# Kernel tuning notes

Hardware: AMD Instinct MI355X
Metric: run time of the kernel (lower is better)

The kernel has to match this reference:

```python
import jax, jax.numpy as jnp
import numpy as np

ACTION_NS = [3, 3, 2, 4, 24]        # forward_back, left_right, jump, sneak_sprint, attack_...
RANGE_STARTS = [6, 8, 10, 11, 14]   # action_ranges starts (indices 0..5 are commit + camera ops)
N_ACTIONS = 37
LOGIT_DIM = 36
MIN_DELTA = 0.5 / 2**3
MAX_STEP = 20
MAX_CAMSTEP = 6
B, NUM_INPUT, HIDDEN = 32768, 1024, 2048
D_IN = NUM_INPUT + 4 + LOGIT_DIM


def setup_inputs():
    key = jax.random.key(0)
    ks = jax.random.split(key, 12)
    inp = {
        "fc_input": jax.random.normal(ks[0], (B, NUM_INPUT), jnp.float32),
        "camera": jax.random.normal(ks[1], (B, 2), jnp.float32),
        "rand_u": jax.random.uniform(ks[2], (B,), jnp.float32),
        "W1": (jax.random.normal(ks[3], (D_IN, HIDDEN), jnp.float32) / np.sqrt(D_IN)).astype(jnp.float32),
        "b1": jnp.zeros((HIDDEN,), jnp.float32),
        "W2": (jax.random.normal(ks[4], (HIDDEN, N_ACTIONS), jnp.float32) / np.sqrt(HIDDEN)).astype(jnp.float32),
        "b2": jnp.zeros((N_ACTIONS,), jnp.float32),
    }
    names = ["act_fb", "act_lr", "act_jp", "act_ss", "act_atk"]
    for i, (nm, n) in enumerate(zip(names, ACTION_NS)):
        inp[nm] = jax.random.randint(ks[5 + i], (B,), 0, n, jnp.int32)
    return inp


def _discretize_scan(camera, acts):
    # Faithful jax version of the 20-step no_grad target/input construction loop.
    nB = camera.shape[0]
    cam0, cam1 = camera[:, 0], camera[:, 1]

    def step(carry, _):
        ac, delta, rdac, dch, cam_steps, committed, norm = carry
        oh = [jax.nn.one_hot(r, n, dtype=jnp.float32) for r, n in zip(rdac, ACTION_NS)]
        inp_vec = jnp.concatenate([ac] + oh + [delta[:, None], dch.astype(jnp.float32)[:, None]], axis=1)  # [B,40]
        norm = norm + (~committed).astype(jnp.float32)
        commit = ((jnp.abs(cam0) < 1e-5) & (jnp.abs(cam1) < 1e-5)) | (cam_steps >= MAX_CAMSTEP)
        for r, a in zip(rdac, acts):
            commit = commit & (r == a)
        dac = jnp.zeros((nB,), jnp.int32)
        modified = commit
        new_rdac = []
        for r, a, rs in zip(rdac, acts, RANGE_STARTS):
            disc = (~modified) & (r != a)
            dac = jnp.where(disc & (a == 0), r - 1 + rs, jnp.where(disc, a - 1 + rs, dac))
            new_rdac.append(jnp.where(disc, a, r))
            modified = modified | disc
        d2 = delta * 2.0
        # NOTE: original torch code compares cam[:,1] against ac[:,0]; bug preserved.
        dmask = (~modified) & (~dch) & ((jnp.abs(cam0 - ac[:, 0]) > d2) | (jnp.abs(cam1 - ac[:, 0]) > d2))
        dac = jnp.where(dmask, 5, dac)
        delta = jnp.where(dmask, jnp.clip(d2, -0.5, 0.5), delta)
        modified = modified | dmask
        sx = jnp.where(cam0 < ac[:, 0], -1.0, 1.0)
        sy = jnp.where(cam1 < ac[:, 1], -1.0, 1.0)
        quad = jnp.where(sx < 0, jnp.where(sy < 0, 1, 3), jnp.where(sy < 0, 2, 4)).astype(jnp.int32)
        dac = jnp.where(~modified, quad, dac)
        move = jnp.stack([sx, sy], axis=1) * delta[:, None]
        ac = jnp.where((~modified)[:, None], ac + move, ac)
        delta = jnp.where(~modified, delta * 0.5, delta)
        dch = dch | (~modified)
        cam_steps = cam_steps + (~modified).astype(jnp.int32)
        committed = committed | commit
        return (ac, delta, tuple(new_rdac), dch, cam_steps, committed, norm), (inp_vec, dac)

    init = (jnp.zeros((nB, 2), jnp.float32),
            jnp.full((nB,), MIN_DELTA, jnp.float32),
            tuple(jnp.zeros((nB,), jnp.int32) for _ in ACTION_NS),
            jnp.zeros((nB,), bool),
            jnp.zeros((nB,), jnp.int32),
            jnp.zeros((nB,), bool),
            jnp.zeros((nB,), jnp.float32))
    carry, (all_inputs, all_dacs) = jax.lax.scan(step, init, None, length=MAX_STEP)
    return all_inputs, all_dacs, carry[-1]  # [T,B,40], [T,B], norm [B]


def reference(fc_input, camera, rand_u, W1, b1, W2, b2, act_fb, act_lr, act_jp, act_ss, act_atk):
    acts = (act_fb, act_lr, act_jp, act_ss, act_atk)
    all_inputs, all_dacs, norm = _discretize_scan(camera, acts)
    rand_sam = jnp.minimum((rand_u * norm).astype(jnp.int32), MAX_STEP - 1)  # sample an uncommitted step
    idx = jnp.arange(fc_input.shape[0])
    sel = jax.lax.stop_gradient(all_inputs[rand_sam, idx])  # [B,40]
    tgt = jax.lax.stop_gradient(all_dacs[rand_sam, idx])    # [B]
    x = jnp.concatenate([fc_input, sel], axis=1)
    h = x @ W1 + b1
    h = h * jax.nn.sigmoid(h)  # swish
    logits = h @ W2 + b2
    logp = jax.nn.log_softmax(logits, axis=-1)
    loss = -jnp.take_along_axis(logp, tgt[:, None], axis=1)[:, 0]  # per-sample CE (reduction='none')
    return loss
```

## Files before the change

kernel.cpp:

```cpp
#include <hip/hip_runtime.h>
#include <hip/hip_bf16.h>
#include <stdint.h>

#define B_ROWS 32768
#define NUM_IN 1024
#define D_PAD2 1088
#define HID    2048
#define NPAD   64

typedef __attribute__((ext_vector_type(8))) short bf16x8;
typedef __attribute__((ext_vector_type(4))) float f32x4;
typedef unsigned short ushort_t;

__device__ __forceinline__ unsigned short f2bf(float f){
  union { float f; uint32_t u; } x; x.f = f;
  uint32_t u = x.u;
  return (unsigned short)((u + 0x7FFFu + ((u >> 16) & 1u)) >> 16);
}

__device__ __forceinline__ void gload16(const void* g, void* l){
  __builtin_amdgcn_global_load_lds((const __attribute__((address_space(1))) void*)g,
                                   (__attribute__((address_space(3))) void*)l, 16, 0, 0);
}

__device__ __forceinline__ int disc_step(
    float cam0, float cam1, const int a[5],
    float& ac0, float& ac1, float& delta,
    int r[5], bool& dch, int& cam_steps, bool& committed, float& norm)
{
  const int RS[5] = {6, 8, 10, 11, 14};
  norm += committed ? 0.0f : 1.0f;
  bool commit = ((fabsf(cam0) < 1e-5f) && (fabsf(cam1) < 1e-5f)) || (cam_steps >= 6);
  #pragma unroll
  for (int i = 0; i < 5; ++i) commit = commit && (r[i] == a[i]);
  int dac = 0;
  bool modified = commit;
  #pragma unroll
  for (int i = 0; i < 5; ++i){
    bool disc = (!modified) && (r[i] != a[i]);
    if (disc){
      dac = (a[i] == 0) ? (r[i] - 1 + RS[i]) : (a[i] - 1 + RS[i]);
      r[i] = a[i];
      modified = true;
    }
  }
  float d2 = delta * 2.0f;
  bool dmask = (!modified) && (!dch) &&
               ((fabsf(cam0 - ac0) > d2) || (fabsf(cam1 - ac0) > d2));
  if (dmask){ dac = 5; delta = fminf(d2, 0.5f); modified = true; }
  if (!modified){
    float sx = (cam0 < ac0) ? -1.0f : 1.0f;
    float sy = (cam1 < ac1) ? -1.0f : 1.0f;
    dac = (sx < 0.0f) ? ((sy < 0.0f) ? 1 : 3) : ((sy < 0.0f) ? 2 : 4);
    ac0 += sx * delta; ac1 += sy * delta;
    delta *= 0.5f;
    dch = true;
    cam_steps += 1;
  }
  committed = committed || commit;
  return dac;
}

__global__ void k_prep(const float* __restrict__ fc, const float* __restrict__ W1,
                       const float* __restrict__ W2,
                       const float* __restrict__ camera, const float* __restrict__ rand_u,
                       const int* __restrict__ afb, const int* __restrict__ alr,
                       const int* __restrict__ ajp, const int* __restrict__ ass,
                       const int* __restrict__ aat,
                       unsigned short* __restrict__ xb, unsigned short* __restrict__ w1t,
                       unsigned short* __restrict__ w2t, int* __restrict__ tgt)
{
  const int b = blockIdx.x;
  const int tid = threadIdx.x;
  if (b < 16384){
    int gid = b * 256 + tid;
    int row = gid >> 7;
    int c   = gid & 127;
    const float4* p = (const float4*)(fc + (size_t)row * NUM_IN + c * 8);
    float4 f0 = p[0], f1 = p[1];
    uint4 pk;
    pk.x = (uint32_t)f2bf(f0.x) | ((uint32_t)f2bf(f0.y) << 16);
    pk.y = (uint32_t)f2bf(f0.z) | ((uint32_t)f2bf(f0.w) << 16);
    pk.z = (uint32_t)f2bf(f1.x) | ((uint32_t)f2bf(f1.y) << 16);
    pk.w = (uint32_t)f2bf(f1.z) | ((uint32_t)f2bf(f1.w) << 16);
    *(uint4*)(xb + (size_t)row * D_PAD2 + c * 8) = pk;
    return;
  }
  if (b < 25088){
    int idx = (b - 16384) * 256 + tid;
    int n = idx / D_PAD2;
    int k = idx - n * D_PAD2;
    float v = (k < 1064) ? W1[(size_t)k * HID + n] : 0.0f;
    w1t[idx] = f2bf(v);
    return;
  }
  if (b < 25600){
    int idx = (b - 25088) * 256 + tid;
    int n = idx >> 11;
    int k = idx & (HID - 1);
    float v = (n < 37) ? W2[(size_t)k * 37 + n] : 0.0f;
    w2t[idx] = f2bf(v);
    return;
  }
  int row = (b - 25600) * 256 + tid;
  float cam0 = camera[2*row], cam1 = camera[2*row + 1];
  int a[5] = { afb[row], alr[row], ajp[row], ass[row], aat[row] };

  float ac0 = 0.f, ac1 = 0.f, delta = 0.0625f, norm = 0.f;
  int r[5] = {0,0,0,0,0};
  bool dch = false, committed = false; int cam_steps = 0;
  for (int t = 0; t < 20; ++t)
    disc_step(cam0, cam1, a, ac0, ac1, delta, r, dch, cam_steps, committed, norm);

  int rs = (int)(rand_u[row] * norm);
  if (rs > 19) rs = 19;
  if (rs < 0) rs = 0;

  ac0 = 0.f; ac1 = 0.f; delta = 0.0625f; norm = 0.f;
  r[0]=r[1]=r[2]=r[3]=r[4]=0; dch = false; committed = false; cam_steps = 0;
  for (int t = 0; t < rs; ++t)
    disc_step(cam0, cam1, a, ac0, ac1, delta, r, dch, cam_steps, committed, norm);

  float vec[40];
  #pragma unroll
  for (int j = 0; j < 40; ++j) vec[j] = 0.0f;
  vec[0] = ac0; vec[1] = ac1;
  const int offs[5] = {2, 5, 8, 10, 14};
  #pragma unroll
  for (int i = 0; i < 5; ++i) vec[offs[i] + r[i]] = 1.0f;
  vec[38] = delta; vec[39] = dch ? 1.0f : 0.0f;

  int dac = disc_step(cam0, cam1, a, ac0, ac1, delta, r, dch, cam_steps, committed, norm);
  tgt[row] = dac;

  unsigned short* o = xb + (size_t)row * D_PAD2 + NUM_IN;
  #pragma unroll
  for (int j = 0; j < 40; ++j) o[j] = f2bf(vec[j]);
  #pragma unroll
  for (int j = 40; j < 64; ++j) o[j] = 0;
}

#define LDS_A0 0
#define LDS_A1 16384
#define LDS_B0 32768
#define LDS_B1 49152

#define STAGE(G, REG, ROW0, KT, HALF) do { \
    const ushort_t* s0_ = (G) + (size_t)((ROW0) + (HALF)*128 + srow) * D_PAD2 + ((KT) << 6) + scol; \
    gload16(s0_, lds + (REG) + (HALF)*8192 + t*8); \
    gload16(s0_ + (size_t)64 * D_PAD2, lds + (REG) + (HALF)*8192 + 4096 + t*8); \
  } while(0)

#define LDA_(REG, MH) do { \
    _Pragma("unroll") for (int mi_ = 0; mi_ < 4; ++mi_){ \
      const int row_ = arow_base + (MH)*64 + mi_*16; \
      _Pragma("unroll") for (int kk_ = 0; kk_ < 2; ++kk_) \
        aR[mi_][kk_] = *(const bf16x8*)(lds + (REG) + row_*64 + (((kk_*4+lg)^axor)<<3)); \
    } \
  } while(0)

#define LDB_(REG, NH, BR) do { \
    _Pragma("unroll") for (int ni_ = 0; ni_ < 2; ++ni_){ \
      const int row_ = brow_base + (NH)*32 + ni_*16; \
      _Pragma("unroll") for (int kk_ = 0; kk_ < 2; ++kk_) \
        BR[ni_][kk_] = *(const bf16x8*)(lds + (REG) + row_*64 + (((kk_*4+lg)^axor)<<3)); \
    } \
  } while(0)

#define MMA(MH, NH, BR) do { \
    __builtin_amdgcn_s_setprio(1); \
    _Pragma("unroll") for (int mi_ = 0; mi_ < 4; ++mi_) \
    _Pragma("unroll") for (int ni_ = 0; ni_ < 2; ++ni_) \
    _Pragma("unroll") for (int kk_ = 0; kk_ < 2; ++kk_) \
      acc[(MH)*4+mi_][(NH)*2+ni_] = __builtin_amdgcn_mfma_f32_16x16x32_bf16( \
          aR[mi_][kk_], BR[ni_][kk_], acc[(MH)*4+mi_][(NH)*2+ni_], 0, 0, 0); \
    __builtin_amdgcn_s_setprio(0); \
  } while(0)

#define BAR() __builtin_amdgcn_s_barrier()
#define WAIT_LGKM0() asm volatile("s_waitcnt lgkmcnt(0)" ::: "memory")
#define WAIT_VM6()   asm volatile("s_waitcnt vmcnt(6)" ::: "memory")
#define WAIT_VM0()   asm volatile("s_waitcnt vmcnt(0)" ::: "memory")

__global__ __launch_bounds__(512, 2) void k_gemm1(const ushort_t* __restrict__ xb,
                                                  const ushort_t* __restrict__ w1t,
                                                  const ushort_t* __restrict__ w2t,
                                                  const float* __restrict__ b1,
                                                  float* __restrict__ pbuf)
{
  __shared__ ushort_t lds[65536];
  const int t = threadIdx.x;
  const int lane = t & 63;
  const int wid = t >> 6, wm = wid >> 2, wn = wid & 3;
  const int lr = lane & 15, lg = lane >> 4;

  const int bid = blockIdx.x;
  const int swz = (bid & 7) * 128 + (bid >> 3);
  const int brow = (swz >> 3) << 8;
  const int bcol = (swz & 7) << 8;

  const int srow = t >> 3;
  const int scol = ((t & 7) ^ (srow & 7)) << 3;

  const int axor = lr & 7;
  const int arow_base = wm*128 + lr;
  const int brow_base = wn*64 + lr;

  f32x4 acc[8][4] = {};
  bf16x8 aR[4][2], bR0[2][2], bR1[2][2];

  STAGE(xb,  LDS_A0, brow, 0, 0);  STAGE(xb,  LDS_A0, brow, 0, 1);
  STAGE(w1t, LDS_B0, bcol, 0, 0);  STAGE(w1t, LDS_B0, bcol, 0, 1);
  STAGE(w1t, LDS_B1, bcol, 1, 0);  STAGE(w1t, LDS_B1, bcol, 1, 1);
  STAGE(xb,  LDS_A1, brow, 1, 0);
  WAIT_VM6();
  BAR();

  for (int i = 0; i < 8; ++i){
    const int c1 = 2*i + 1;
    const int n0 = 2*i + 2;
    const int n1 = (2*i + 3 <= 16) ? 2*i + 3 : 16;

    LDA_(LDS_A0, 0); LDB_(LDS_B0, 0, bR0); LDB_(LDS_B0, 1, bR1);
    STAGE(xb, LDS_A1, brow, c1, 1);
    BAR(); WAIT_LGKM0();
    MMA(0, 0, bR0);
    BAR();
    STAGE(w1t, LDS_B0, bcol, n0, 0);
    BAR();
    MMA(0, 1, bR1);
    BAR();
    LDA_(LDS_A0, 1);
    STAGE(w1t, LDS_B0, bcol, n0, 1);
    BAR(); WAIT_LGKM0();
    MMA(1, 0, bR0);
    BAR();
    STAGE(xb, LDS_A0, brow, n0, 0);
    WAIT_VM6();
    BAR();
    MMA(1, 1, bR1);
    BAR();
    LDA_(LDS_A1, 0); LDB_(LDS_B1, 0, bR0); LDB_(LDS_B1, 1, bR1);
    STAGE(xb, LDS_A0, brow, n0, 1);
    BAR(); WAIT_LGKM0();
    MMA(0, 0, bR0);
    BAR();
    STAGE(w1t, LDS_B1, bcol, n1, 0);
    BAR();
    MMA(0, 1, bR1);
    BAR();
    LDA_(LDS_A1, 1);
    STAGE(w1t, LDS_B1, bcol, n1, 1);
    BAR(); WAIT_LGKM0();
    MMA(1, 0, bR0);
    BAR();
    STAGE(xb, LDS_A1, brow, n1, 0);
    WAIT_VM6();
    BAR();
    MMA(1, 1, bR1);
    BAR();
  }

  LDA_(LDS_A0, 0); LDB_(LDS_B0, 0, bR0); LDB_(LDS_B0, 1, bR1);
  MMA(0, 0, bR0); MMA(0, 1, bR1);
  LDA_(LDS_A0, 1);
  MMA(1, 0, bR0); MMA(1, 1, bR1);

  bf16x8 w2fA[4][4];
  #pragma unroll
  for (int ks = 0; ks < 4; ++ks)
    #pragma unroll
    for (int ni = 0; ni < 4; ++ni)
      w2fA[ks][ni] = *(const bf16x8*)(w2t + (size_t)(ni*16 + lr) * HID + bcol + ks*32 + lg*8);

  WAIT_VM0();
  BAR();

  float b1v[4];
  #pragma unroll
  for (int ni = 0; ni < 4; ++ni) b1v[ni] = b1[bcol + wn*64 + ni*16 + lr];

  #pragma unroll
  for (int mi = 0; mi < 8; ++mi){
    #pragma unroll
    for (int ni = 0; ni < 4; ++ni){
      const int col = wn*64 + ni*16 + lr;
      #pragma unroll
      for (int i2 = 0; i2 < 4; ++i2){
        const int row = wm*128 + mi*16 + lg*4 + i2;
        float v = acc[mi][ni][i2] + b1v[ni];
        float s = v / (1.0f + __expf(-v));
        const int chunk = (col >> 3) ^ (row & 7);
        lds[row*256 + chunk*8 + (col & 7)] = f2bf(s);
      }
    }
  }
  __syncthreads();

  bf16x8 w2fB[4][4];
  #pragma unroll
  for (int ks = 0; ks < 4; ++ks)
    #pragma unroll
    for (int ni = 0; ni < 4; ++ni)
      w2fB[ks][ni] = *(const bf16x8*)(w2t + (size_t)(ni*16 + lr) * HID + bcol + (ks+4)*32 + lg*8);

  const int rb = wid * 32;
  f32x4 acc2[2][4] = {};
  #pragma unroll
  for (int ks = 0; ks < 8; ++ks){
    bf16x8 a2[2];
    #pragma unroll
    for (int m = 0; m < 2; ++m){
      const int row = rb + m*16 + lr;
      a2[m] = *(const bf16x8*)(lds + row*256 + (((ks*4+lg) ^ (lr & 7)) << 3));
    }
    #pragma unroll
    for (int m = 0; m < 2; ++m)
      #pragma unroll
      for (int ni = 0; ni < 4; ++ni)
        acc2[m][ni] = __builtin_amdgcn_mfma_f32_16x16x32_bf16(
            a2[m], (ks < 4) ? w2fA[ks & 3][ni] : w2fB[ks & 3][ni], acc2[m][ni], 0, 0, 0);
  }

  const int cb = bcol >> 8;
  #pragma unroll
  for (int m = 0; m < 2; ++m)
    #pragma unroll
    for (int ni = 0; ni < 4; ++ni)
      #pragma unroll
      for (int i2 = 0; i2 < 4; ++i2){
        const int r = brow + rb + m*16 + lg*4 + i2;
        pbuf[((size_t)cb << 21) + ((size_t)r << 6) + ni*16 + lr] = acc2[m][ni][i2];
      }
}

__global__ __launch_bounds__(256) void k_red(const float* __restrict__ pbuf,
                                             const float* __restrict__ b2,
                                             const int* __restrict__ tgt,
                                             float* __restrict__ loss)
{
  const int lane = threadIdx.x & 63, w = threadIdx.x >> 6;
  const int row0 = blockIdx.x * 128 + w * 32;
  const float bias = (lane < 37) ? b2[lane] : 0.0f;
  for (int i = 0; i < 32; ++i){
    const int r = row0 + i;
    float s = 0.0f;
    #pragma unroll
    for (int cb = 0; cb < 8; ++cb)
      s += pbuf[((size_t)cb << 21) + ((size_t)r << 6) + lane];
    float x = (lane < 37) ? (s + bias) : -1e30f;
    float m = x;
    #pragma unroll
    for (int off = 1; off < 64; off <<= 1) m = fmaxf(m, __shfl_xor(m, off, 64));
    float e = __expf(x - m);
    float se = e;
    #pragma unroll
    for (int off = 1; off < 64; off <<= 1) se += __shfl_xor(se, off, 64);
    const int tg = tgt[r];
    const float pick = __shfl(x, tg, 64);
    if (lane == 0) loss[r] = m + __logf(se) - pick;
  }
}

extern "C" void kernel_launch(void* const* d_in, const int* in_sizes, int n_in,
                              void* d_out, int out_size, void* d_ws, size_t ws_size,
                              hipStream_t stream)
{
  (void)in_sizes; (void)n_in; (void)out_size; (void)ws_size;
  const float* fc  = (const float*)d_in[0];
  const float* cam = (const float*)d_in[1];
  const float* ru  = (const float*)d_in[2];
  const float* W1  = (const float*)d_in[3];
  const float* b1  = (const float*)d_in[4];
  const float* W2  = (const float*)d_in[5];
  const float* b2  = (const float*)d_in[6];
  const int* afb = (const int*)d_in[7];
  const int* alr = (const int*)d_in[8];
  const int* ajp = (const int*)d_in[9];
  const int* ass = (const int*)d_in[10];
  const int* aat = (const int*)d_in[11];
  float* loss = (float*)d_out;

  char* ws = (char*)d_ws;
  unsigned short* xb  = (unsigned short*)(ws);
  unsigned short* w1t = (unsigned short*)(ws + 71303168);
  unsigned short* w2t = (unsigned short*)(ws + 75759616);
  int*            tgt = (int*)           (ws + 76021760);
  float*          pbuf= (float*)         (ws + 76152832);

  k_prep<<<25728, 256, 0, stream>>>(fc, W1, W2, cam, ru, afb, alr, ajp, ass, aat,
                                    xb, w1t, w2t, tgt);
  k_gemm1<<<(B_ROWS/256) * (HID/256), 512, 0, stream>>>(xb, w1t, w2t, b1, pbuf);
  k_red  <<<B_ROWS / 128, 256, 0, stream>>>(pbuf, b2, tgt, loss);
}
```

Baseline: 275.6 us.

## Double-buffer GEMM1 register fragments to overlap LDS reads with MFMA

Splits the A and B operand registers into two banks and issues the LDS fragment reads for the next sub-tile before the current MFMA block runs. This replaces the explicit lgkmcnt(0) waits, so LDS read latency can hide behind matrix math, and the epilogue is reordered to match. The cost is many more live VGPRs under a 512-thread, 2-block launch bound, which risks register spills or lower occupancy. Correctness now depends on the compiler inserting the right waits before each fragment is used.

```diff
diff --git a/kernel.cpp b/kernel.cpp
--- a/kernel.cpp
+++ b/kernel.cpp
@@ -151,34 +151,34 @@
     gload16(s0_ + (size_t)64 * D_PAD2, lds + (REG) + (HALF)*8192 + 4096 + t*8); \
   } while(0)
 
-#define LDA_(REG, MH) do { \
+#define RDA(BANK, REG, MH) do { \
     _Pragma("unroll") for (int mi_ = 0; mi_ < 4; ++mi_){ \
       const int row_ = arow_base + (MH)*64 + mi_*16; \
       _Pragma("unroll") for (int kk_ = 0; kk_ < 2; ++kk_) \
-        aR[mi_][kk_] = *(const bf16x8*)(lds + (REG) + row_*64 + (((kk_*4+lg)^axor)<<3)); \
+        BANK[mi_][kk_] = *(const bf16x8*)(lds + (REG) + row_*64 + (((kk_*4+lg)^axor)<<3)); \
     } \
   } while(0)
 
-#define LDB_(REG, NH, BR) do { \
+#define RDB(BANK, REG) do { \
+    _Pragma("unroll") for (int nh_ = 0; nh_ < 2; ++nh_) \
     _Pragma("unroll") for (int ni_ = 0; ni_ < 2; ++ni_){ \
-      const int row_ = brow_base + (NH)*32 + ni_*16; \
+      const int row_ = brow_base + nh_*32 + ni_*16; \
       _Pragma("unroll") for (int kk_ = 0; kk_ < 2; ++kk_) \
-        BR[ni_][kk_] = *(const bf16x8*)(lds + (REG) + row_*64 + (((kk_*4+lg)^axor)<<3)); \
+        BANK[nh_][ni_][kk_] = *(const bf16x8*)(lds + (REG) + row_*64 + (((kk_*4+lg)^axor)<<3)); \
     } \
   } while(0)
 
-#define MMA(MH, NH, BR) do { \
+#define MMAQ(AB, MH, BB, NH) do { \
     __builtin_amdgcn_s_setprio(1); \
     _Pragma("unroll") for (int mi_ = 0; mi_ < 4; ++mi_) \
     _Pragma("unroll") for (int ni_ = 0; ni_ < 2; ++ni_) \
     _Pragma("unroll") for (int kk_ = 0; kk_ < 2; ++kk_) \
       acc[(MH)*4+mi_][(NH)*2+ni_] = __builtin_amdgcn_mfma_f32_16x16x32_bf16( \
-          aR[mi_][kk_], BR[ni_][kk_], acc[(MH)*4+mi_][(NH)*2+ni_], 0, 0, 0); \
+          AB[mi_][kk_], BB[NH][ni_][kk_], acc[(MH)*4+mi_][(NH)*2+ni_], 0, 0, 0); \
     __builtin_amdgcn_s_setprio(0); \
   } while(0)
 
 #define BAR() __builtin_amdgcn_s_barrier()
-#define WAIT_LGKM0() asm volatile("s_waitcnt lgkmcnt(0)" ::: "memory")
 #define WAIT_VM6()   asm volatile("s_waitcnt vmcnt(6)" ::: "memory")
 #define WAIT_VM0()   asm volatile("s_waitcnt vmcnt(0)" ::: "memory")
 
@@ -207,7 +207,7 @@
   const int brow_base = wn*64 + lr;
 
   f32x4 acc[8][4] = {};
-  bf16x8 aR[4][2], bR0[2][2], bR1[2][2];
+  bf16x8 aA[4][2], aB[4][2], bX[2][2][2], bY[2][2][2];
 
   STAGE(xb,  LDS_A0, brow, 0, 0);  STAGE(xb,  LDS_A0, brow, 0, 1);
   STAGE(w1t, LDS_B0, bcol, 0, 0);  STAGE(w1t, LDS_B0, bcol, 0, 1);
@@ -215,56 +215,58 @@
   STAGE(xb,  LDS_A1, brow, 1, 0);
   WAIT_VM6();
   BAR();
+  RDA(aA, LDS_A0, 0); RDB(bX, LDS_B0);
 
   for (int i = 0; i < 8; ++i){
     const int c1 = 2*i + 1;
     const int n0 = 2*i + 2;
     const int n1 = (2*i + 3 <= 16) ? 2*i + 3 : 16;
 
-    LDA_(LDS_A0, 0); LDB_(LDS_B0, 0, bR0); LDB_(LDS_B0, 1, bR1);
     STAGE(xb, LDS_A1, brow, c1, 1);
-    BAR(); WAIT_LGKM0();
-    MMA(0, 0, bR0);
+    BAR();
+    RDA(aB, LDS_A0, 1);
+    MMAQ(aA, 0, bX, 0);
     BAR();
     STAGE(w1t, LDS_B0, bcol, n0, 0);
     BAR();
-    MMA(0, 1, bR1);
-    BAR();
-    LDA_(LDS_A0, 1);
+    MMAQ(aA, 0, bX, 1);
+    BAR();
     STAGE(w1t, LDS_B0, bcol, n0, 1);
-    BAR(); WAIT_LGKM0();
-    MMA(1, 0, bR0);
+    BAR();
+    MMAQ(aB, 1, bX, 0);
     BAR();
     STAGE(xb, LDS_A0, brow, n0, 0);
     WAIT_VM6();
     BAR();
-    MMA(1, 1, bR1);
-    BAR();
-    LDA_(LDS_A1, 0); LDB_(LDS_B1, 0, bR0); LDB_(LDS_B1, 1, bR1);
+    RDA(aA, LDS_A1, 0); RDB(bY, LDS_B1);
+    MMAQ(aB, 1, bX, 1);
+    BAR();
     STAGE(xb, LDS_A0, brow, n0, 1);
-    BAR(); WAIT_LGKM0();
-    MMA(0, 0, bR0);
+    BAR();
+    RDA(aB, LDS_A1, 1);
+    MMAQ(aA, 0, bY, 0);
     BAR();
     STAGE(w1t, LDS_B1, bcol, n1, 0);
     BAR();
-    MMA(0, 1, bR1);
-    BAR();
-    LDA_(LDS_A1, 1);
+    MMAQ(aA, 0, bY, 1);
+    BAR();
     STAGE(w1t, LDS_B1, bcol, n1, 1);
-    BAR(); WAIT_LGKM0();
-    MMA(1, 0, bR0);
+    BAR();
+    MMAQ(aB, 1, bY, 0);
     BAR();
     STAGE(xb, LDS_A1, brow, n1, 0);
     WAIT_VM6();
     BAR();
-    MMA(1, 1, bR1);
-    BAR();
-  }
-
-  LDA_(LDS_A0, 0); LDB_(LDS_B0, 0, bR0); LDB_(LDS_B0, 1, bR1);
-  MMA(0, 0, bR0); MMA(0, 1, bR1);
-  LDA_(LDS_A0, 1);
-  MMA(1, 0, bR0); MMA(1, 1, bR1);
+    RDA(aA, LDS_A0, 0); RDB(bX, LDS_B0);
+    MMAQ(aB, 1, bY, 1);
+    BAR();
+  }
+
+  MMAQ(aA, 0, bX, 0);
+  RDA(aB, LDS_A0, 1);
+  MMAQ(aA, 0, bX, 1);
+  MMAQ(aB, 1, bX, 0);
+  MMAQ(aB, 1, bX, 1);
 
   bf16x8 w2fA[4][4];
   #pragma unroll
```

After: 527.0 us. +91.2%, slower.
